# Optimization experiments

Measured on AMD Instinct MI355X. Metric: run time of the kernel, lower is better.

Reference implementation:

```python
import math
import jax, jax.numpy as jnp
import numpy as np

R, K, H = 512, 250, 4      # num_ranges, top-K per range, heads
E = 16                     # embed_dim*2 (MHA width), head_dim = 4
LN_EPS = 1e-5


def _layernorm(x, g, b):
    mu = jnp.mean(x, axis=-1, keepdims=True)
    var = jnp.mean(jnp.square(x - mu), axis=-1, keepdims=True)
    return (x - mu) * jax.lax.rsqrt(var + LN_EPS) * g + b


def setup_inputs() -> dict:
    key = jax.random.key(0)
    ks = jax.random.split(key, 12)
    L = 2  # num_layers
    s = 0.02
    return {
        "power_vals": jax.random.normal(ks[0], (R * K, 8), jnp.float32),
        "ele_indices": jax.random.randint(ks[1], (R * K,), 0, 37),
        "azi_indices": jax.random.randint(ks[2], (R * K,), 0, 107),
        "vp_w": jax.random.normal(ks[3], (8, 8), jnp.float32) * s,      # values_project: Linear(8, embed_dim=8)
        "vp_b": jnp.zeros((8,), jnp.float32),
        "ele_emb": jax.random.normal(ks[4], (37, 4), jnp.float32) * s,  # Embedding(37, embed_dim//2)
        "azi_emb": jax.random.normal(ks[5], (107, 4), jnp.float32) * s, # Embedding(107, embed_dim//2)
        "in_proj_w": jax.random.normal(ks[6], (L, 3 * E, E), jnp.float32) * s,
        "in_proj_b": jnp.zeros((L, 3 * E), jnp.float32),
        "out_w": jax.random.normal(ks[7], (L, E, E), jnp.float32) * s,
        "out_b": jnp.zeros((L, E), jnp.float32),
        "ln_g": jnp.ones((E,), jnp.float32),
        "ln_b": jnp.zeros((E,), jnp.float32),
    }


def reference(power_vals, ele_indices, azi_indices, vp_w, vp_b, ele_emb, azi_emb,
              in_proj_w, in_proj_b, out_w, out_b, ln_g, ln_b):
    D = E // H
    scale = 1.0 / math.sqrt(D)
    pv = power_vals.reshape(R, K, 8)
    top_values = pv @ vp_w.T + vp_b                      # [R,K,8]
    ele = ele_emb[ele_indices.reshape(R, K)]             # [R,K,4]
    azi = azi_emb[azi_indices.reshape(R, K)]             # [R,K,4]
    x = jnp.concatenate([top_values, ele, azi], axis=-1) # [R,K,16]

    # eval mode: dropout (both in MHA and after norm) is identity
    for l in range(in_proj_w.shape[0]):
        qkv = x @ in_proj_w[l].T + in_proj_b[l]          # [R,K,48]
        q, k, v = jnp.split(qkv, 3, axis=-1)
        q = q.reshape(R, K, H, D) * scale
        k = k.reshape(R, K, H, D)
        v = v.reshape(R, K, H, D)
        att = jnp.einsum('rqhd,rkhd->rhqk', q, k)        # [R,H,K,K]
        p = jax.nn.softmax(att, axis=-1)
        o = jnp.einsum('rhqk,rkhd->rqhd', p, v).reshape(R, K, E)
        o = o @ out_w[l].T + out_b[l]                    # out_proj
        x = _layernorm(o + x, ln_g, ln_b)                # shared LayerNorm, residual
    return x.reshape(R * K, E)
```

## Files before the change

### kernel.cpp

```cpp
#include <hip/hip_runtime.h>

#define R_ 512
#define K_ 250
#define E_ 16
#define L_ 2
#define SX_S 20

#define SCALE_LOG2E 0.72134752044448170f

#define ATT_STEP(KP, VP) do {                                                        \
    const float4 k0 = ((const float4*)(KP))[0];                                      \
    const float4 k1 = ((const float4*)(KP))[1];                                      \
    const float4 k2 = ((const float4*)(KP))[2];                                      \
    const float4 k3 = ((const float4*)(KP))[3];                                      \
    float s00 = fmaf(q0[0],k0.x, fmaf(q0[1],k0.y, fmaf(q0[2],k0.z, q0[3]*k0.w)));    \
    float s01 = fmaf(q0[4],k1.x, fmaf(q0[5],k1.y, fmaf(q0[6],k1.z, q0[7]*k1.w)));    \
    float s02 = fmaf(q0[8],k2.x, fmaf(q0[9],k2.y, fmaf(q0[10],k2.z, q0[11]*k2.w)));  \
    float s03 = fmaf(q0[12],k3.x, fmaf(q0[13],k3.y, fmaf(q0[14],k3.z, q0[15]*k3.w)));\
    float s10 = fmaf(q1[0],k0.x, fmaf(q1[1],k0.y, fmaf(q1[2],k0.z, q1[3]*k0.w)));    \
    float s11 = fmaf(q1[4],k1.x, fmaf(q1[5],k1.y, fmaf(q1[6],k1.z, q1[7]*k1.w)));    \
    float s12 = fmaf(q1[8],k2.x, fmaf(q1[9],k2.y, fmaf(q1[10],k2.z, q1[11]*k2.w)));  \
    float s13 = fmaf(q1[12],k3.x, fmaf(q1[13],k3.y, fmaf(q1[14],k3.z, q1[15]*k3.w)));\
    const float p00 = __builtin_amdgcn_exp2f(s00);                                   \
    const float p01 = __builtin_amdgcn_exp2f(s01);                                   \
    const float p02 = __builtin_amdgcn_exp2f(s02);                                   \
    const float p03 = __builtin_amdgcn_exp2f(s03);                                   \
    const float p10 = __builtin_amdgcn_exp2f(s10);                                   \
    const float p11 = __builtin_amdgcn_exp2f(s11);                                   \
    const float p12 = __builtin_amdgcn_exp2f(s12);                                   \
    const float p13 = __builtin_amdgcn_exp2f(s13);                                   \
    const float4 v0 = ((const float4*)(VP))[0];                                      \
    const float4 v1 = ((const float4*)(VP))[1];                                      \
    const float4 v2 = ((const float4*)(VP))[2];                                      \
    const float4 v3 = ((const float4*)(VP))[3];                                      \
    ls0 += p00; ls1 += p01; ls2 += p02; ls3 += p03;                                  \
    ls4 += p10; ls5 += p11; ls6 += p12; ls7 += p13;                                  \
    acc0[0]  = fmaf(p00, v0.x, acc0[0]);  acc0[1]  = fmaf(p00, v0.y, acc0[1]);       \
    acc0[2]  = fmaf(p00, v0.z, acc0[2]);  acc0[3]  = fmaf(p00, v0.w, acc0[3]);       \
    acc0[4]  = fmaf(p01, v1.x, acc0[4]);  acc0[5]  = fmaf(p01, v1.y, acc0[5]);       \
    acc0[6]  = fmaf(p01, v1.z, acc0[6]);  acc0[7]  = fmaf(p01, v1.w, acc0[7]);       \
    acc0[8]  = fmaf(p02, v2.x, acc0[8]);  acc0[9]  = fmaf(p02, v2.y, acc0[9]);       \
    acc0[10] = fmaf(p02, v2.z, acc0[10]); acc0[11] = fmaf(p02, v2.w, acc0[11]);      \
    acc0[12] = fmaf(p03, v3.x, acc0[12]); acc0[13] = fmaf(p03, v3.y, acc0[13]);      \
    acc0[14] = fmaf(p03, v3.z, acc0[14]); acc0[15] = fmaf(p03, v3.w, acc0[15]);      \
    acc1[0]  = fmaf(p10, v0.x, acc1[0]);  acc1[1]  = fmaf(p10, v0.y, acc1[1]);       \
    acc1[2]  = fmaf(p10, v0.z, acc1[2]);  acc1[3]  = fmaf(p10, v0.w, acc1[3]);       \
    acc1[4]  = fmaf(p11, v1.x, acc1[4]);  acc1[5]  = fmaf(p11, v1.y, acc1[5]);       \
    acc1[6]  = fmaf(p11, v1.z, acc1[6]);  acc1[7]  = fmaf(p11, v1.w, acc1[7]);       \
    acc1[8]  = fmaf(p12, v2.x, acc1[8]);  acc1[9]  = fmaf(p12, v2.y, acc1[9]);       \
    acc1[10] = fmaf(p12, v2.z, acc1[10]); acc1[11] = fmaf(p12, v2.w, acc1[11]);      \
    acc1[12] = fmaf(p13, v3.x, acc1[12]); acc1[13] = fmaf(p13, v3.y, acc1[13]);      \
    acc1[14] = fmaf(p13, v3.z, acc1[14]); acc1[15] = fmaf(p13, v3.w, acc1[15]);      \
} while (0)

__global__ __launch_bounds__(512, 2)
void mlra_kernel(const float* __restrict__ pv,
                 const int*   __restrict__ ele_idx,
                 const int*   __restrict__ azi_idx,
                 const float* __restrict__ vp_w,
                 const float* __restrict__ vp_b,
                 const float* __restrict__ ele_emb,
                 const float* __restrict__ azi_emb,
                 const float* __restrict__ ipw,
                 const float* __restrict__ ipb,
                 const float* __restrict__ outw,
                 const float* __restrict__ outb,
                 const float* __restrict__ lng,
                 const float* __restrict__ lnb,
                 float* __restrict__ out)
{
    __shared__ float s_k[K_][16];
    __shared__ float s_v[K_][16];
    __shared__ float s_x[K_][SX_S];
    __shared__ float s_w[768];
    __shared__ float s_b[48];
    __shared__ float s_ow[256];
    __shared__ float s_ob[16];
    __shared__ float s_vpw[64];
    __shared__ float s_vpb[8];
    __shared__ float s_ele[148];
    __shared__ float s_azi[428];
    __shared__ float s_lng[16], s_lnb[16];

    const int r = blockIdx.x;
    const int t = threadIdx.x;

    if (t < 64) s_vpw[t] = vp_w[t];
    if (t < 8)  s_vpb[t] = vp_b[t];
    for (int i = t; i < 148; i += 512) s_ele[i] = ele_emb[i];
    for (int i = t; i < 428; i += 512) s_azi[i] = azi_emb[i];
    if (t < 16) { s_lng[t] = lng[t]; s_lnb[t] = lnb[t]; }
    __syncthreads();

    if (t < K_) {
        const size_t row = (size_t)r * K_ + t;
        const float4 p0 = ((const float4*)(pv + row * 8))[0];
        const float4 p1 = ((const float4*)(pv + row * 8))[1];
        const float a[8] = {p0.x,p0.y,p0.z,p0.w,p1.x,p1.y,p1.z,p1.w};
        float xr[16];
        #pragma unroll
        for (int o = 0; o < 8; ++o) {
            const float4 w0 = ((const float4*)&s_vpw[o*8])[0];
            const float4 w1 = ((const float4*)&s_vpw[o*8])[1];
            float s = s_vpb[o];
            s = fmaf(a[0],w0.x,s); s = fmaf(a[1],w0.y,s); s = fmaf(a[2],w0.z,s); s = fmaf(a[3],w0.w,s);
            s = fmaf(a[4],w1.x,s); s = fmaf(a[5],w1.y,s); s = fmaf(a[6],w1.z,s); s = fmaf(a[7],w1.w,s);
            xr[o] = s;
        }
        const int ei = ele_idx[row];
        const int ai = azi_idx[row];
        const float4 ee = *(const float4*)&s_ele[ei*4];
        const float4 ae = *(const float4*)&s_azi[ai*4];
        xr[8]=ee.x; xr[9]=ee.y; xr[10]=ee.z; xr[11]=ee.w;
        xr[12]=ae.x; xr[13]=ae.y; xr[14]=ae.z; xr[15]=ae.w;
        float4* xd = (float4*)&s_x[t][0];
        xd[0] = make_float4(xr[0],xr[1],xr[2],xr[3]);
        xd[1] = make_float4(xr[4],xr[5],xr[6],xr[7]);
        xd[2] = make_float4(xr[8],xr[9],xr[10],xr[11]);
        xd[3] = make_float4(xr[12],xr[13],xr[14],xr[15]);
    }

    const int  qp      = t >> 2;
    const int  quarter = t & 3;
    const bool act     = qp < 125;
    const int  q0row   = 2*qp;
    const int  q1row   = 2*qp + 1;
    const int  od      = 4*quarter;

    for (int l = 0; l < L_; ++l) {
        __syncthreads();
        for (int i = t; i < 768; i += 512) s_w[i] = ipw[l*768 + i];
        if (t < 48)  s_b[t]  = ipb[l*48 + t];
        if (t < 256) s_ow[t] = outw[l*256 + t];
        if (t < 16)  s_ob[t] = outb[l*16 + t];
        __syncthreads();

        float q0[16], q1[16];
        if (act) {
            float x0[16], x1[16];
            {
                const float4* xa = (const float4*)&s_x[q0row][0];
                const float4 a0 = xa[0], a1 = xa[1], a2 = xa[2], a3 = xa[3];
                x0[0]=a0.x; x0[1]=a0.y; x0[2]=a0.z; x0[3]=a0.w;
                x0[4]=a1.x; x0[5]=a1.y; x0[6]=a1.z; x0[7]=a1.w;
                x0[8]=a2.x; x0[9]=a2.y; x0[10]=a2.z; x0[11]=a2.w;
                x0[12]=a3.x; x0[13]=a3.y; x0[14]=a3.z; x0[15]=a3.w;
                const float4* xb = (const float4*)&s_x[q1row][0];
                const float4 b0 = xb[0], b1 = xb[1], b2 = xb[2], b3 = xb[3];
                x1[0]=b0.x; x1[1]=b0.y; x1[2]=b0.z; x1[3]=b0.w;
                x1[4]=b1.x; x1[5]=b1.y; x1[6]=b1.z; x1[7]=b1.w;
                x1[8]=b2.x; x1[9]=b2.y; x1[10]=b2.z; x1[11]=b2.w;
                x1[12]=b3.x; x1[13]=b3.y; x1[14]=b3.z; x1[15]=b3.w;
            }
            #pragma unroll
            for (int o = 0; o < 16; ++o) {
                const float4 w0 = ((const float4*)&s_w[o*16])[0];
                const float4 w1 = ((const float4*)&s_w[o*16])[1];
                const float4 w2 = ((const float4*)&s_w[o*16])[2];
                const float4 w3 = ((const float4*)&s_w[o*16])[3];
                const float b = s_b[o];
                float a0 = b, a1 = b;
                a0=fmaf(x0[0],w0.x,a0); a0=fmaf(x0[1],w0.y,a0); a0=fmaf(x0[2],w0.z,a0); a0=fmaf(x0[3],w0.w,a0);
                a0=fmaf(x0[4],w1.x,a0); a0=fmaf(x0[5],w1.y,a0); a0=fmaf(x0[6],w1.z,a0); a0=fmaf(x0[7],w1.w,a0);
                a0=fmaf(x0[8],w2.x,a0); a0=fmaf(x0[9],w2.y,a0); a0=fmaf(x0[10],w2.z,a0); a0=fmaf(x0[11],w2.w,a0);
                a0=fmaf(x0[12],w3.x,a0); a0=fmaf(x0[13],w3.y,a0); a0=fmaf(x0[14],w3.z,a0); a0=fmaf(x0[15],w3.w,a0);
                a1=fmaf(x1[0],w0.x,a1); a1=fmaf(x1[1],w0.y,a1); a1=fmaf(x1[2],w0.z,a1); a1=fmaf(x1[3],w0.w,a1);
                a1=fmaf(x1[4],w1.x,a1); a1=fmaf(x1[5],w1.y,a1); a1=fmaf(x1[6],w1.z,a1); a1=fmaf(x1[7],w1.w,a1);
                a1=fmaf(x1[8],w2.x,a1); a1=fmaf(x1[9],w2.y,a1); a1=fmaf(x1[10],w2.z,a1); a1=fmaf(x1[11],w2.w,a1);
                a1=fmaf(x1[12],w3.x,a1); a1=fmaf(x1[13],w3.y,a1); a1=fmaf(x1[14],w3.z,a1); a1=fmaf(x1[15],w3.w,a1);
                q0[o] = a0 * SCALE_LOG2E;
                q1[o] = a1 * SCALE_LOG2E;
            }
            float xs[16];
            #pragma unroll
            for (int i = 0; i < 16; ++i) xs[i] = (quarter & 1) ? x1[i] : x0[i];
            const int kvb = (quarter < 2) ? 16 : 32;
            float kv[16];
            #pragma unroll
            for (int o = 0; o < 16; ++o) {
                const float* wr = &s_w[(kvb + o)*16];
                const float4 w0 = ((const float4*)wr)[0];
                const float4 w1 = ((const float4*)wr)[1];
                const float4 w2 = ((const float4*)wr)[2];
                const float4 w3 = ((const float4*)wr)[3];
                float s = s_b[kvb + o];
                s=fmaf(xs[0],w0.x,s); s=fmaf(xs[1],w0.y,s); s=fmaf(xs[2],w0.z,s); s=fmaf(xs[3],w0.w,s);
                s=fmaf(xs[4],w1.x,s); s=fmaf(xs[5],w1.y,s); s=fmaf(xs[6],w1.z,s); s=fmaf(xs[7],w1.w,s);
                s=fmaf(xs[8],w2.x,s); s=fmaf(xs[9],w2.y,s); s=fmaf(xs[10],w2.z,s); s=fmaf(xs[11],w2.w,s);
                s=fmaf(xs[12],w3.x,s); s=fmaf(xs[13],w3.y,s); s=fmaf(xs[14],w3.z,s); s=fmaf(xs[15],w3.w,s);
                kv[o] = s;
            }
            float* dst = ((quarter < 2) ? &s_k[0][0] : &s_v[0][0]) + (q0row + (quarter & 1))*16;
            ((float4*)dst)[0] = make_float4(kv[0],kv[1],kv[2],kv[3]);
            ((float4*)dst)[1] = make_float4(kv[4],kv[5],kv[6],kv[7]);
            ((float4*)dst)[2] = make_float4(kv[8],kv[9],kv[10],kv[11]);
            ((float4*)dst)[3] = make_float4(kv[12],kv[13],kv[14],kv[15]);
        }
        __syncthreads();

        if (act) {
            float acc0[16], acc1[16];
            #pragma unroll
            for (int i = 0; i < 16; ++i) { acc0[i] = 0.0f; acc1[i] = 0.0f; }
            float ls0=0.f, ls1=0.f, ls2=0.f, ls3=0.f, ls4=0.f, ls5=0.f, ls6=0.f, ls7=0.f;

            const float* kp  = &s_k[quarter][0];
            const float* vp2 = &s_v[quarter][0];
            #pragma unroll 2
            for (int jj = 0; jj < 62; ++jj) {
                ATT_STEP(kp, vp2);
                kp += 64; vp2 += 64;
            }
            if (quarter < 2) {
                ATT_STEP(kp, vp2);
            }

            #pragma unroll
            for (int i = 0; i < 16; ++i) {
                acc0[i] += __shfl_xor(acc0[i], 1);
                acc1[i] += __shfl_xor(acc1[i], 1);
            }
            ls0 += __shfl_xor(ls0,1); ls1 += __shfl_xor(ls1,1);
            ls2 += __shfl_xor(ls2,1); ls3 += __shfl_xor(ls3,1);
            ls4 += __shfl_xor(ls4,1); ls5 += __shfl_xor(ls5,1);
            ls6 += __shfl_xor(ls6,1); ls7 += __shfl_xor(ls7,1);
            #pragma unroll
            for (int i = 0; i < 16; ++i) {
                acc0[i] += __shfl_xor(acc0[i], 2);
                acc1[i] += __shfl_xor(acc1[i], 2);
            }
            ls0 += __shfl_xor(ls0,2); ls1 += __shfl_xor(ls1,2);
            ls2 += __shfl_xor(ls2,2); ls3 += __shfl_xor(ls3,2);
            ls4 += __shfl_xor(ls4,2); ls5 += __shfl_xor(ls5,2);
            ls6 += __shfl_xor(ls6,2); ls7 += __shfl_xor(ls7,2);

            const float i00 = __builtin_amdgcn_rcpf(ls0);
            const float i01 = __builtin_amdgcn_rcpf(ls1);
            const float i02 = __builtin_amdgcn_rcpf(ls2);
            const float i03 = __builtin_amdgcn_rcpf(ls3);
            const float i10 = __builtin_amdgcn_rcpf(ls4);
            const float i11 = __builtin_amdgcn_rcpf(ls5);
            const float i12 = __builtin_amdgcn_rcpf(ls6);
            const float i13 = __builtin_amdgcn_rcpf(ls7);
            float o0[16], o1[16];
            o0[0]=acc0[0]*i00;  o0[1]=acc0[1]*i00;  o0[2]=acc0[2]*i00;  o0[3]=acc0[3]*i00;
            o0[4]=acc0[4]*i01;  o0[5]=acc0[5]*i01;  o0[6]=acc0[6]*i01;  o0[7]=acc0[7]*i01;
            o0[8]=acc0[8]*i02;  o0[9]=acc0[9]*i02;  o0[10]=acc0[10]*i02; o0[11]=acc0[11]*i02;
            o0[12]=acc0[12]*i03; o0[13]=acc0[13]*i03; o0[14]=acc0[14]*i03; o0[15]=acc0[15]*i03;
            o1[0]=acc1[0]*i10;  o1[1]=acc1[1]*i10;  o1[2]=acc1[2]*i10;  o1[3]=acc1[3]*i10;
            o1[4]=acc1[4]*i11;  o1[5]=acc1[5]*i11;  o1[6]=acc1[6]*i11;  o1[7]=acc1[7]*i11;
            o1[8]=acc1[8]*i12;  o1[9]=acc1[9]*i12;  o1[10]=acc1[10]*i12; o1[11]=acc1[11]*i12;
            o1[12]=acc1[12]*i13; o1[13]=acc1[13]*i13; o1[14]=acc1[14]*i13; o1[15]=acc1[15]*i13;

            float y0[4], y1[4];
            #pragma unroll
            for (int c = 0; c < 4; ++c) {
                const float* wr = &s_ow[(od + c)*16];
                const float4 w0 = ((const float4*)wr)[0];
                const float4 w1 = ((const float4*)wr)[1];
                const float4 w2 = ((const float4*)wr)[2];
                const float4 w3 = ((const float4*)wr)[3];
                const float b = s_ob[od + c];
                float a0 = b, a1 = b;
                a0=fmaf(o0[0],w0.x,a0); a0=fmaf(o0[1],w0.y,a0); a0=fmaf(o0[2],w0.z,a0); a0=fmaf(o0[3],w0.w,a0);
                a0=fmaf(o0[4],w1.x,a0); a0=fmaf(o0[5],w1.y,a0); a0=fmaf(o0[6],w1.z,a0); a0=fmaf(o0[7],w1.w,a0);
                a0=fmaf(o0[8],w2.x,a0); a0=fmaf(o0[9],w2.y,a0); a0=fmaf(o0[10],w2.z,a0); a0=fmaf(o0[11],w2.w,a0);
                a0=fmaf(o0[12],w3.x,a0); a0=fmaf(o0[13],w3.y,a0); a0=fmaf(o0[14],w3.z,a0); a0=fmaf(o0[15],w3.w,a0);
                a1=fmaf(o1[0],w0.x,a1); a1=fmaf(o1[1],w0.y,a1); a1=fmaf(o1[2],w0.z,a1); a1=fmaf(o1[3],w0.w,a1);
                a1=fmaf(o1[4],w1.x,a1); a1=fmaf(o1[5],w1.y,a1); a1=fmaf(o1[6],w1.z,a1); a1=fmaf(o1[7],w1.w,a1);
                a1=fmaf(o1[8],w2.x,a1); a1=fmaf(o1[9],w2.y,a1); a1=fmaf(o1[10],w2.z,a1); a1=fmaf(o1[11],w2.w,a1);
                a1=fmaf(o1[12],w3.x,a1); a1=fmaf(o1[13],w3.y,a1); a1=fmaf(o1[14],w3.z,a1); a1=fmaf(o1[15],w3.w,a1);
                y0[c] = a0; y1[c] = a1;
            }
            const float4 xr0 = *(const float4*)&s_x[q0row][od];
            const float4 xr1 = *(const float4*)&s_x[q1row][od];
            const float t00 = y0[0]+xr0.x, t01 = y0[1]+xr0.y, t02 = y0[2]+xr0.z, t03 = y0[3]+xr0.w;
            const float t10 = y1[0]+xr1.x, t11 = y1[1]+xr1.y, t12 = y1[2]+xr1.z, t13 = y1[3]+xr1.w;
            float sum0 = (t00+t01)+(t02+t03);
            float sq0  = fmaf(t00,t00, fmaf(t01,t01, fmaf(t02,t02, t03*t03)));
            float sum1 = (t10+t11)+(t12+t13);
            float sq1  = fmaf(t10,t10, fmaf(t11,t11, fmaf(t12,t12, t13*t13)));
            sum0 += __shfl_xor(sum0,1); sum0 += __shfl_xor(sum0,2);
            sq0  += __shfl_xor(sq0,1);  sq0  += __shfl_xor(sq0,2);
            sum1 += __shfl_xor(sum1,1); sum1 += __shfl_xor(sum1,2);
            sq1  += __shfl_xor(sq1,1);  sq1  += __shfl_xor(sq1,2);
            const float mu0 = sum0 * 0.0625f;
            const float mu1 = sum1 * 0.0625f;
            const float var0 = fmaf(-mu0, mu0, sq0 * 0.0625f);
            const float var1 = fmaf(-mu1, mu1, sq1 * 0.0625f);
            const float rs0 = __builtin_amdgcn_rsqf(var0 + 1e-5f);
            const float rs1 = __builtin_amdgcn_rsqf(var1 + 1e-5f);
            const float4 g  = *(const float4*)&s_lng[od];
            const float4 bb = *(const float4*)&s_lnb[od];
            float4 xn0, xn1;
            xn0.x = (t00-mu0)*rs0*g.x + bb.x;  xn0.y = (t01-mu0)*rs0*g.y + bb.y;
            xn0.z = (t02-mu0)*rs0*g.z + bb.z;  xn0.w = (t03-mu0)*rs0*g.w + bb.w;
            xn1.x = (t10-mu1)*rs1*g.x + bb.x;  xn1.y = (t11-mu1)*rs1*g.y + bb.y;
            xn1.z = (t12-mu1)*rs1*g.z + bb.z;  xn1.w = (t13-mu1)*rs1*g.w + bb.w;
            *(float4*)&s_x[q0row][od] = xn0;
            *(float4*)&s_x[q1row][od] = xn1;
            if (l == L_ - 1) {
                float* ob = out + ((size_t)r*K_ + q0row)*16 + od;
                *(float4*)ob        = xn0;
                *(float4*)(ob + 16) = xn1;
            }
        }
    }
}

extern "C" void kernel_launch(void* const* d_in, const int* in_sizes, int n_in,
                              void* d_out, int out_size, void* d_ws, size_t ws_size,
                              hipStream_t stream) {
    const float* pv      = (const float*)d_in[0];
    const int*   ele_idx = (const int*)  d_in[1];
    const int*   azi_idx = (const int*)  d_in[2];
    const float* vp_w    = (const float*)d_in[3];
    const float* vp_b    = (const float*)d_in[4];
    const float* ele_emb = (const float*)d_in[5];
    const float* azi_emb = (const float*)d_in[6];
    const float* ipw     = (const float*)d_in[7];
    const float* ipb     = (const float*)d_in[8];
    const float* outw    = (const float*)d_in[9];
    const float* outb    = (const float*)d_in[10];
    const float* lng     = (const float*)d_in[11];
    const float* lnb     = (const float*)d_in[12];
    float* out = (float*)d_out;

    mlra_kernel<<<R_, 512, 0, stream>>>(pv, ele_idx, azi_idx, vp_w, vp_b,
                                        ele_emb, azi_emb, ipw, ipb,
                                        outw, outb, lng, lnb, out);
}
```

Before: 189.1 us.

## Split layers into two launches, each range split across two blocks

The single fused kernel, with one block per range looping over both layers, becomes two templated launches, one per layer, passing activations through a workspace buffer. Each range now gets two blocks that each own half the queries, and both blocks recompute K and V for the whole range. Eight threads share each query pair instead of four, with a wider shuffle reduction. This raises block count and per-query parallelism at the cost of redundant K/V projection, an extra global round trip for the activations, and a second launch.

```diff
diff --git a/kernel.cpp b/kernel.cpp
--- a/kernel.cpp
+++ b/kernel.cpp
@@ -2,10 +2,7 @@
 
 #define R_ 512
 #define K_ 250
-#define E_ 16
-#define L_ 2
-#define SX_S 20
-
+#define SK 20
 #define SCALE_LOG2E 0.72134752044448170f
 
 #define ATT_STEP(KP, VP) do {                                                        \
@@ -53,25 +50,27 @@
     acc1[14] = fmaf(p13, v3.z, acc1[14]); acc1[15] = fmaf(p13, v3.w, acc1[15]);      \
 } while (0)
 
+template<int PASS>
 __global__ __launch_bounds__(512, 2)
-void mlra_kernel(const float* __restrict__ pv,
-                 const int*   __restrict__ ele_idx,
-                 const int*   __restrict__ azi_idx,
-                 const float* __restrict__ vp_w,
-                 const float* __restrict__ vp_b,
-                 const float* __restrict__ ele_emb,
-                 const float* __restrict__ azi_emb,
-                 const float* __restrict__ ipw,
-                 const float* __restrict__ ipb,
-                 const float* __restrict__ outw,
-                 const float* __restrict__ outb,
-                 const float* __restrict__ lng,
-                 const float* __restrict__ lnb,
-                 float* __restrict__ out)
+void mlra_pass(const float* __restrict__ pv,
+               const int*   __restrict__ ele_idx,
+               const int*   __restrict__ azi_idx,
+               const float* __restrict__ vp_w,
+               const float* __restrict__ vp_b,
+               const float* __restrict__ ele_emb,
+               const float* __restrict__ azi_emb,
+               const float* __restrict__ ipw,
+               const float* __restrict__ ipb,
+               const float* __restrict__ outw,
+               const float* __restrict__ outb,
+               const float* __restrict__ lng,
+               const float* __restrict__ lnb,
+               const float* __restrict__ xin,
+               float* __restrict__ xout)
 {
-    __shared__ float s_k[K_][16];
-    __shared__ float s_v[K_][16];
-    __shared__ float s_x[K_][SX_S];
+    __shared__ float s_k[K_][SK];
+    __shared__ float s_v[K_][SK];
+    __shared__ float s_x[252][SK];
     __shared__ float s_w[768];
     __shared__ float s_b[48];
     __shared__ float s_ow[256];
@@ -82,228 +81,238 @@
     __shared__ float s_azi[428];
     __shared__ float s_lng[16], s_lnb[16];
 
-    const int r = blockIdx.x;
+    const int r = blockIdx.x >> 1;
+    const int s = blockIdx.x & 1;
     const int t = threadIdx.x;
 
-    if (t < 64) s_vpw[t] = vp_w[t];
-    if (t < 8)  s_vpb[t] = vp_b[t];
-    for (int i = t; i < 148; i += 512) s_ele[i] = ele_emb[i];
-    for (int i = t; i < 428; i += 512) s_azi[i] = azi_emb[i];
-    if (t < 16) { s_lng[t] = lng[t]; s_lnb[t] = lnb[t]; }
+    for (int i = t; i < 768; i += 512) s_w[i] = ipw[PASS*768 + i];
+    if (t < 48)  s_b[t]  = ipb[PASS*48 + t];
+    if (t < 256) s_ow[t] = outw[PASS*256 + t];
+    if (t < 16)  s_ob[t] = outb[PASS*16 + t];
+    if (t < 16)  { s_lng[t] = lng[t]; s_lnb[t] = lnb[t]; }
+    if (PASS == 0) {
+        if (t >= 64 && t < 128) s_vpw[t-64] = vp_w[t-64];
+        if (t >= 128 && t < 136) s_vpb[t-128] = vp_b[t-128];
+        for (int i = t; i < 148; i += 512) s_ele[i] = ele_emb[i];
+        for (int i = t; i < 428; i += 512) s_azi[i] = azi_emb[i];
+    }
     __syncthreads();
 
     if (t < K_) {
-        const size_t row = (size_t)r * K_ + t;
-        const float4 p0 = ((const float4*)(pv + row * 8))[0];
-        const float4 p1 = ((const float4*)(pv + row * 8))[1];
-        const float a[8] = {p0.x,p0.y,p0.z,p0.w,p1.x,p1.y,p1.z,p1.w};
         float xr[16];
-        #pragma unroll
-        for (int o = 0; o < 8; ++o) {
-            const float4 w0 = ((const float4*)&s_vpw[o*8])[0];
-            const float4 w1 = ((const float4*)&s_vpw[o*8])[1];
-            float s = s_vpb[o];
-            s = fmaf(a[0],w0.x,s); s = fmaf(a[1],w0.y,s); s = fmaf(a[2],w0.z,s); s = fmaf(a[3],w0.w,s);
-            s = fmaf(a[4],w1.x,s); s = fmaf(a[5],w1.y,s); s = fmaf(a[6],w1.z,s); s = fmaf(a[7],w1.w,s);
-            xr[o] = s;
-        }
-        const int ei = ele_idx[row];
-        const int ai = azi_idx[row];
-        const float4 ee = *(const float4*)&s_ele[ei*4];
-        const float4 ae = *(const float4*)&s_azi[ai*4];
-        xr[8]=ee.x; xr[9]=ee.y; xr[10]=ee.z; xr[11]=ee.w;
-        xr[12]=ae.x; xr[13]=ae.y; xr[14]=ae.z; xr[15]=ae.w;
+        if (PASS == 0) {
+            const size_t row = (size_t)r * K_ + t;
+            const float4 p0 = ((const float4*)(pv + row * 8))[0];
+            const float4 p1 = ((const float4*)(pv + row * 8))[1];
+            const float a[8] = {p0.x,p0.y,p0.z,p0.w,p1.x,p1.y,p1.z,p1.w};
+            #pragma unroll
+            for (int o = 0; o < 8; ++o) {
+                const float4 w0 = ((const float4*)&s_vpw[o*8])[0];
+                const float4 w1 = ((const float4*)&s_vpw[o*8])[1];
+                float sv = s_vpb[o];
+                sv = fmaf(a[0],w0.x,sv); sv = fmaf(a[1],w0.y,sv); sv = fmaf(a[2],w0.z,sv); sv = fmaf(a[3],w0.w,sv);
+                sv = fmaf(a[4],w1.x,sv); sv = fmaf(a[5],w1.y,sv); sv = fmaf(a[6],w1.z,sv); sv = fmaf(a[7],w1.w,sv);
+                xr[o] = sv;
+            }
+            const int ei = ele_idx[row];
+            const int ai = azi_idx[row];
+            const float4 ee = *(const float4*)&s_ele[ei*4];
+            const float4 ae = *(const float4*)&s_azi[ai*4];
+            xr[8]=ee.x; xr[9]=ee.y; xr[10]=ee.z; xr[11]=ee.w;
+            xr[12]=ae.x; xr[13]=ae.y; xr[14]=ae.z; xr[15]=ae.w;
+        } else {
+            const float4* src = (const float4*)(xin + ((size_t)r * K_ + t) * 16);
+            const float4 a0 = src[0], a1 = src[1], a2 = src[2], a3 = src[3];
+            xr[0]=a0.x; xr[1]=a0.y; xr[2]=a0.z; xr[3]=a0.w;
+            xr[4]=a1.x; xr[5]=a1.y; xr[6]=a1.z; xr[7]=a1.w;
+            xr[8]=a2.x; xr[9]=a2.y; xr[10]=a2.z; xr[11]=a2.w;
+            xr[12]=a3.x; xr[13]=a3.y; xr[14]=a3.z; xr[15]=a3.w;
+        }
         float4* xd = (float4*)&s_x[t][0];
         xd[0] = make_float4(xr[0],xr[1],xr[2],xr[3]);
         xd[1] = make_float4(xr[4],xr[5],xr[6],xr[7]);
         xd[2] = make_float4(xr[8],xr[9],xr[10],xr[11]);
         xd[3] = make_float4(xr[12],xr[13],xr[14],xr[15]);
-    }
-
-    const int  qp      = t >> 2;
-    const int  quarter = t & 3;
-    const bool act     = qp < 125;
-    const int  q0row   = 2*qp;
-    const int  q1row   = 2*qp + 1;
-    const int  od      = 4*quarter;
-
-    for (int l = 0; l < L_; ++l) {
-        __syncthreads();
-        for (int i = t; i < 768; i += 512) s_w[i] = ipw[l*768 + i];
-        if (t < 48)  s_b[t]  = ipb[l*48 + t];
-        if (t < 256) s_ow[t] = outw[l*256 + t];
-        if (t < 16)  s_ob[t] = outb[l*16 + t];
-        __syncthreads();
-
-        float q0[16], q1[16];
-        if (act) {
-            float x0[16], x1[16];
-            {
-                const float4* xa = (const float4*)&s_x[q0row][0];
-                const float4 a0 = xa[0], a1 = xa[1], a2 = xa[2], a3 = xa[3];
-                x0[0]=a0.x; x0[1]=a0.y; x0[2]=a0.z; x0[3]=a0.w;
-                x0[4]=a1.x; x0[5]=a1.y; x0[6]=a1.z; x0[7]=a1.w;
-                x0[8]=a2.x; x0[9]=a2.y; x0[10]=a2.z; x0[11]=a2.w;
-                x0[12]=a3.x; x0[13]=a3.y; x0[14]=a3.z; x0[15]=a3.w;
-                const float4* xb = (const float4*)&s_x[q1row][0];
-                const float4 b0 = xb[0], b1 = xb[1], b2 = xb[2], b3 = xb[3];
-                x1[0]=b0.x; x1[1]=b0.y; x1[2]=b0.z; x1[3]=b0.w;
-                x1[4]=b1.x; x1[5]=b1.y; x1[6]=b1.z; x1[7]=b1.w;
-                x1[8]=b2.x; x1[9]=b2.y; x1[10]=b2.z; x1[11]=b2.w;
-                x1[12]=b3.x; x1[13]=b3.y; x1[14]=b3.z; x1[15]=b3.w;
-            }
-            #pragma unroll
-            for (int o = 0; o < 16; ++o) {
-                const float4 w0 = ((const float4*)&s_w[o*16])[0];
-                const float4 w1 = ((const float4*)&s_w[o*16])[1];
-                const float4 w2 = ((const float4*)&s_w[o*16])[2];
-                const float4 w3 = ((const float4*)&s_w[o*16])[3];
-                const float b = s_b[o];
-                float a0 = b, a1 = b;
-                a0=fmaf(x0[0],w0.x,a0); a0=fmaf(x0[1],w0.y,a0); a0=fmaf(x0[2],w0.z,a0); a0=fmaf(x0[3],w0.w,a0);
-                a0=fmaf(x0[4],w1.x,a0); a0=fmaf(x0[5],w1.y,a0); a0=fmaf(x0[6],w1.z,a0); a0=fmaf(x0[7],w1.w,a0);
-                a0=fmaf(x0[8],w2.x,a0); a0=fmaf(x0[9],w2.y,a0); a0=fmaf(x0[10],w2.z,a0); a0=fmaf(x0[11],w2.w,a0);
-                a0=fmaf(x0[12],w3.x,a0); a0=fmaf(x0[13],w3.y,a0); a0=fmaf(x0[14],w3.z,a0); a0=fmaf(x0[15],w3.w,a0);
-                a1=fmaf(x1[0],w0.x,a1); a1=fmaf(x1[1],w0.y,a1); a1=fmaf(x1[2],w0.z,a1); a1=fmaf(x1[3],w0.w,a1);
-                a1=fmaf(x1[4],w1.x,a1); a1=fmaf(x1[5],w1.y,a1); a1=fmaf(x1[6],w1.z,a1); a1=fmaf(x1[7],w1.w,a1);
-                a1=fmaf(x1[8],w2.x,a1); a1=fmaf(x1[9],w2.y,a1); a1=fmaf(x1[10],w2.z,a1); a1=fmaf(x1[11],w2.w,a1);
-                a1=fmaf(x1[12],w3.x,a1); a1=fmaf(x1[13],w3.y,a1); a1=fmaf(x1[14],w3.z,a1); a1=fmaf(x1[15],w3.w,a1);
-                q0[o] = a0 * SCALE_LOG2E;
-                q1[o] = a1 * SCALE_LOG2E;
-            }
-            float xs[16];
-            #pragma unroll
-            for (int i = 0; i < 16; ++i) xs[i] = (quarter & 1) ? x1[i] : x0[i];
-            const int kvb = (quarter < 2) ? 16 : 32;
+    } else if (t < 252 + 6) {
+        if (t >= 256 && t < 258) {
+            float4* xd = (float4*)&s_x[250 + (t - 256)][0];
+            xd[0] = xd[1] = xd[2] = xd[3] = make_float4(0.f,0.f,0.f,0.f);
+        }
+    }
+    __syncthreads();
+
+    const int  qp    = t >> 3;
+    const int  e     = t & 7;
+    const bool qact  = qp < 63;
+    const int  qbase = s * 125;
+    const int  arow  = qbase + 2*qp;
+    const int  brow  = arow + 1;
+    const bool bval  = brow < K_;
+    const int  od    = 2*e;
+
+    float q0[16], q1[16];
+    if (qact) {
+        float x0[16], x1[16];
+        {
+            const float4* xa = (const float4*)&s_x[arow][0];
+            const float4 a0 = xa[0], a1 = xa[1], a2 = xa[2], a3 = xa[3];
+            x0[0]=a0.x; x0[1]=a0.y; x0[2]=a0.z; x0[3]=a0.w;
+            x0[4]=a1.x; x0[5]=a1.y; x0[6]=a1.z; x0[7]=a1.w;
+            x0[8]=a2.x; x0[9]=a2.y; x0[10]=a2.z; x0[11]=a2.w;
+            x0[12]=a3.x; x0[13]=a3.y; x0[14]=a3.z; x0[15]=a3.w;
+            const float4* xb = (const float4*)&s_x[brow][0];
+            const float4 b0 = xb[0], b1 = xb[1], b2 = xb[2], b3 = xb[3];
+            x1[0]=b0.x; x1[1]=b0.y; x1[2]=b0.z; x1[3]=b0.w;
+            x1[4]=b1.x; x1[5]=b1.y; x1[6]=b1.z; x1[7]=b1.w;
+            x1[8]=b2.x; x1[9]=b2.y; x1[10]=b2.z; x1[11]=b2.w;
+            x1[12]=b3.x; x1[13]=b3.y; x1[14]=b3.z; x1[15]=b3.w;
+        }
+        #pragma unroll
+        for (int o = 0; o < 16; ++o) {
+            const float4 w0 = ((const float4*)&s_w[o*16])[0];
+            const float4 w1 = ((const float4*)&s_w[o*16])[1];
+            const float4 w2 = ((const float4*)&s_w[o*16])[2];
+            const float4 w3 = ((const float4*)&s_w[o*16])[3];
+            const float b = s_b[o];
+            float a0 = b, a1 = b;
+            a0=fmaf(x0[0],w0.x,a0); a0=fmaf(x0[1],w0.y,a0); a0=fmaf(x0[2],w0.z,a0); a0=fmaf(x0[3],w0.w,a0);
+            a0=fmaf(x0[4],w1.x,a0); a0=fmaf(x0[5],w1.y,a0); a0=fmaf(x0[6],w1.z,a0); a0=fmaf(x0[7],w1.w,a0);
+            a0=fmaf(x0[8],w2.x,a0); a0=fmaf(x0[9],w2.y,a0); a0=fmaf(x0[10],w2.z,a0); a0=fmaf(x0[11],w2.w,a0);
+            a0=fmaf(x0[12],w3.x,a0); a0=fmaf(x0[13],w3.y,a0); a0=fmaf(x0[14],w3.z,a0); a0=fmaf(x0[15],w3.w,a0);
+            a1=fmaf(x1[0],w0.x,a1); a1=fmaf(x1[1],w0.y,a1); a1=fmaf(x1[2],w0.z,a1); a1=fmaf(x1[3],w0.w,a1);
+            a1=fmaf(x1[4],w1.x,a1); a1=fmaf(x1[5],w1.y,a1); a1=fmaf(x1[6],w1.z,a1); a1=fmaf(x1[7],w1.w,a1);
+            a1=fmaf(x1[8],w2.x,a1); a1=fmaf(x1[9],w2.y,a1); a1=fmaf(x1[10],w2.z,a1); a1=fmaf(x1[11],w2.w,a1);
+            a1=fmaf(x1[12],w3.x,a1); a1=fmaf(x1[13],w3.y,a1); a1=fmaf(x1[14],w3.z,a1); a1=fmaf(x1[15],w3.w,a1);
+            q0[o] = a0 * SCALE_LOG2E;
+            q1[o] = a1 * SCALE_LOG2E;
+        }
+    }
+    {
+        int kvrow = -1, base = 16;
+        if (t < K_)                        { kvrow = t;       base = 16; }
+        else if (t >= 256 && t < 256 + K_) { kvrow = t - 256; base = 32; }
+        if (kvrow >= 0) {
+            const float4* xs4 = (const float4*)&s_x[kvrow][0];
+            const float4 a0 = xs4[0], a1 = xs4[1], a2 = xs4[2], a3 = xs4[3];
+            const float xs[16] = {a0.x,a0.y,a0.z,a0.w, a1.x,a1.y,a1.z,a1.w,
+                                  a2.x,a2.y,a2.z,a2.w, a3.x,a3.y,a3.z,a3.w};
             float kv[16];
             #pragma unroll
             for (int o = 0; o < 16; ++o) {
-                const float* wr = &s_w[(kvb + o)*16];
+                const float* wr = &s_w[(base + o)*16];
                 const float4 w0 = ((const float4*)wr)[0];
                 const float4 w1 = ((const float4*)wr)[1];
                 const float4 w2 = ((const float4*)wr)[2];
                 const float4 w3 = ((const float4*)wr)[3];
-                float s = s_b[kvb + o];
-                s=fmaf(xs[0],w0.x,s); s=fmaf(xs[1],w0.y,s); s=fmaf(xs[2],w0.z,s); s=fmaf(xs[3],w0.w,s);
-                s=fmaf(xs[4],w1.x,s); s=fmaf(xs[5],w1.y,s); s=fmaf(xs[6],w1.z,s); s=fmaf(xs[7],w1.w,s);
-                s=fmaf(xs[8],w2.x,s); s=fmaf(xs[9],w2.y,s); s=fmaf(xs[10],w2.z,s); s=fmaf(xs[11],w2.w,s);
-                s=fmaf(xs[12],w3.x,s); s=fmaf(xs[13],w3.y,s); s=fmaf(xs[14],w3.z,s); s=fmaf(xs[15],w3.w,s);
-                kv[o] = s;
+                float sv = s_b[base + o];
+                sv=fmaf(xs[0],w0.x,sv); sv=fmaf(xs[1],w0.y,sv); sv=fmaf(xs[2],w0.z,sv); sv=fmaf(xs[3],w0.w,sv);
+                sv=fmaf(xs[4],w1.x,sv); sv=fmaf(xs[5],w1.y,sv); sv=fmaf(xs[6],w1.z,sv); sv=fmaf(xs[7],w1.w,sv);
+                sv=fmaf(xs[8],w2.x,sv); sv=fmaf(xs[9],w2.y,sv); sv=fmaf(xs[10],w2.z,sv); sv=fmaf(xs[11],w2.w,sv);
+                sv=fmaf(xs[12],w3.x,sv); sv=fmaf(xs[13],w3.y,sv); sv=fmaf(xs[14],w3.z,sv); sv=fmaf(xs[15],w3.w,sv);
+                kv[o] = sv;
             }
-            float* dst = ((quarter < 2) ? &s_k[0][0] : &s_v[0][0]) + (q0row + (quarter & 1))*16;
+            float* dst = (base == 16) ? &s_k[kvrow][0] : &s_v[kvrow][0];
             ((float4*)dst)[0] = make_float4(kv[0],kv[1],kv[2],kv[3]);
             ((float4*)dst)[1] = make_float4(kv[4],kv[5],kv[6],kv[7]);
             ((float4*)dst)[2] = make_float4(kv[8],kv[9],kv[10],kv[11]);
             ((float4*)dst)[3] = make_float4(kv[12],kv[13],kv[14],kv[15]);
         }
-        __syncthreads();
-
-        if (act) {
-            float acc0[16], acc1[16];
-            #pragma unroll
-            for (int i = 0; i < 16; ++i) { acc0[i] = 0.0f; acc1[i] = 0.0f; }
-            float ls0=0.f, ls1=0.f, ls2=0.f, ls3=0.f, ls4=0.f, ls5=0.f, ls6=0.f, ls7=0.f;
-
-            const float* kp  = &s_k[quarter][0];
-            const float* vp2 = &s_v[quarter][0];
-            #pragma unroll 2
-            for (int jj = 0; jj < 62; ++jj) {
-                ATT_STEP(kp, vp2);
-                kp += 64; vp2 += 64;
-            }
-            if (quarter < 2) {
-                ATT_STEP(kp, vp2);
-            }
-
+    }
+    __syncthreads();
+
+    if (qact) {
+        float acc0[16], acc1[16];
+        #pragma unroll
+        for (int i = 0; i < 16; ++i) { acc0[i] = 0.0f; acc1[i] = 0.0f; }
+        float ls0=0.f, ls1=0.f, ls2=0.f, ls3=0.f, ls4=0.f, ls5=0.f, ls6=0.f, ls7=0.f;
+
+        const float* kp  = &s_k[e][0];
+        const float* vp2 = &s_v[e][0];
+        const int n = 31 + ((e < 2) ? 1 : 0);
+        #pragma unroll 2
+        for (int jj = 0; jj < n; ++jj) {
+            ATT_STEP(kp, vp2);
+            kp += 8*SK; vp2 += 8*SK;
+        }
+
+        #pragma unroll
+        for (int m = 1; m <= 4; m <<= 1) {
             #pragma unroll
             for (int i = 0; i < 16; ++i) {
-                acc0[i] += __shfl_xor(acc0[i], 1);
-                acc1[i] += __shfl_xor(acc1[i], 1);
+                acc0[i] += __shfl_xor(acc0[i], m);
+                acc1[i] += __shfl_xor(acc1[i], m);
             }
-            ls0 += __shfl_xor(ls0,1); ls1 += __shfl_xor(ls1,1);
-            ls2 += __shfl_xor(ls2,1); ls3 += __shfl_xor(ls3,1);
-            ls4 += __shfl_xor(ls4,1); ls5 += __shfl_xor(ls5,1);
-            ls6 += __shfl_xor(ls6,1); ls7 += __shfl_xor(ls7,1);
-            #pragma unroll
-            for (int i = 0; i < 16; ++i) {
-                acc0[i] += __shfl_xor(acc0[i], 2);
-                acc1[i] += __shfl_xor(acc1[i], 2);
-            }
-            ls0 += __shfl_xor(ls0,2); ls1 += __shfl_xor(ls1,2);
-            ls2 += __shfl_xor(ls2,2); ls3 += __shfl_xor(ls3,2);
-            ls4 += __shfl_xor(ls4,2); ls5 += __shfl_xor(ls5,2);
-            ls6 += __shfl_xor(ls6,2); ls7 += __shfl_xor(ls7,2);
-
-            const float i00 = __builtin_amdgcn_rcpf(ls0);
-            const float i01 = __builtin_amdgcn_rcpf(ls1);
-            const float i02 = __builtin_amdgcn_rcpf(ls2);
-            const float i03 = __builtin_amdgcn_rcpf(ls3);
-            const float i10 = __builtin_amdgcn_rcpf(ls4);
-            const float i11 = __builtin_amdgcn_rcpf(ls5);
-            const float i12 = __builtin_amdgcn_rcpf(ls6);
-            const float i13 = __builtin_amdgcn_rcpf(ls7);
-            float o0[16], o1[16];
-            o0[0]=acc0[0]*i00;  o0[1]=acc0[1]*i00;  o0[2]=acc0[2]*i00;  o0[3]=acc0[3]*i00;
-            o0[4]=acc0[4]*i01;  o0[5]=acc0[5]*i01;  o0[6]=acc0[6]*i01;  o0[7]=acc0[7]*i01;
-            o0[8]=acc0[8]*i02;  o0[9]=acc0[9]*i02;  o0[10]=acc0[10]*i02; o0[11]=acc0[11]*i02;
-            o0[12]=acc0[12]*i03; o0[13]=acc0[13]*i03; o0[14]=acc0[14]*i03; o0[15]=acc0[15]*i03;
-            o1[0]=acc1[0]*i10;  o1[1]=acc1[1]*i10;  o1[2]=acc1[2]*i10;  o1[3]=acc1[3]*i10;
-            o1[4]=acc1[4]*i11;  o1[5]=acc1[5]*i11;  o1[6]=acc1[6]*i11;  o1[7]=acc1[7]*i11;
-            o1[8]=acc1[8]*i12;  o1[9]=acc1[9]*i12;  o1[10]=acc1[10]*i12; o1[11]=acc1[11]*i12;
-            o1[12]=acc1[12]*i13; o1[13]=acc1[13]*i13; o1[14]=acc1[14]*i13; o1[15]=acc1[15]*i13;
-
-            float y0[4], y1[4];
-            #pragma unroll
-            for (int c = 0; c < 4; ++c) {
-                const float* wr = &s_ow[(od + c)*16];
-                const float4 w0 = ((const float4*)wr)[0];
-                const float4 w1 = ((const float4*)wr)[1];
-                const float4 w2 = ((const float4*)wr)[2];
-                const float4 w3 = ((const float4*)wr)[3];
-                const float b = s_ob[od + c];
-                float a0 = b, a1 = b;
-                a0=fmaf(o0[0],w0.x,a0); a0=fmaf(o0[1],w0.y,a0); a0=fmaf(o0[2],w0.z,a0); a0=fmaf(o0[3],w0.w,a0);
-                a0=fmaf(o0[4],w1.x,a0); a0=fmaf(o0[5],w1.y,a0); a0=fmaf(o0[6],w1.z,a0); a0=fmaf(o0[7],w1.w,a0);
-                a0=fmaf(o0[8],w2.x,a0); a0=fmaf(o0[9],w2.y,a0); a0=fmaf(o0[10],w2.z,a0); a0=fmaf(o0[11],w2.w,a0);
-                a0=fmaf(o0[12],w3.x,a0); a0=fmaf(o0[13],w3.y,a0); a0=fmaf(o0[14],w3.z,a0); a0=fmaf(o0[15],w3.w,a0);
-                a1=fmaf(o1[0],w0.x,a1); a1=fmaf(o1[1],w0.y,a1); a1=fmaf(o1[2],w0.z,a1); a1=fmaf(o1[3],w0.w,a1);
-                a1=fmaf(o1[4],w1.x,a1); a1=fmaf(o1[5],w1.y,a1); a1=fmaf(o1[6],w1.z,a1); a1=fmaf(o1[7],w1.w,a1);
-                a1=fmaf(o1[8],w2.x,a1); a1=fmaf(o1[9],w2.y,a1); a1=fmaf(o1[10],w2.z,a1); a1=fmaf(o1[11],w2.w,a1);
-                a1=fmaf(o1[12],w3.x,a1); a1=fmaf(o1[13],w3.y,a1); a1=fmaf(o1[14],w3.z,a1); a1=fmaf(o1[15],w3.w,a1);
-                y0[c] = a0; y1[c] = a1;
-            }
-            const float4 xr0 = *(const float4*)&s_x[q0row][od];
-            const float4 xr1 = *(const float4*)&s_x[q1row][od];
-            const float t00 = y0[0]+xr0.x, t01 = y0[1]+xr0.y, t02 = y0[2]+xr0.z, t03 = y0[3]+xr0.w;
-            const float t10 = y1[0]+xr1.x, t11 = y1[1]+xr1.y, t12 = y1[2]+xr1.z, t13 = y1[3]+xr1.w;
-            float sum0 = (t00+t01)+(t02+t03);
-            float sq0  = fmaf(t00,t00, fmaf(t01,t01, fmaf(t02,t02, t03*t03)));
-            float sum1 = (t10+t11)+(t12+t13);
-            float sq1  = fmaf(t10,t10, fmaf(t11,t11, fmaf(t12,t12, t13*t13)));
-            sum0 += __shfl_xor(sum0,1); sum0 += __shfl_xor(sum0,2);
-            sq0  += __shfl_xor(sq0,1);  sq0  += __shfl_xor(sq0,2);
-            sum1 += __shfl_xor(sum1,1); sum1 += __shfl_xor(sum1,2);
-            sq1  += __shfl_xor(sq1,1);  sq1  += __shfl_xor(sq1,2);
-            const float mu0 = sum0 * 0.0625f;
-            const float mu1 = sum1 * 0.0625f;
-            const float var0 = fmaf(-mu0, mu0, sq0 * 0.0625f);
-            const float var1 = fmaf(-mu1, mu1, sq1 * 0.0625f);
-            const float rs0 = __builtin_amdgcn_rsqf(var0 + 1e-5f);
-            const float rs1 = __builtin_amdgcn_rsqf(var1 + 1e-5f);
-            const float4 g  = *(const float4*)&s_lng[od];
-            const float4 bb = *(const float4*)&s_lnb[od];
-            float4 xn0, xn1;
-            xn0.x = (t00-mu0)*rs0*g.x + bb.x;  xn0.y = (t01-mu0)*rs0*g.y + bb.y;
-            xn0.z = (t02-mu0)*rs0*g.z + bb.z;  xn0.w = (t03-mu0)*rs0*g.w + bb.w;
-            xn1.x = (t10-mu1)*rs1*g.x + bb.x;  xn1.y = (t11-mu1)*rs1*g.y + bb.y;
-            xn1.z = (t12-mu1)*rs1*g.z + bb.z;  xn1.w = (t13-mu1)*rs1*g.w + bb.w;
-            *(float4*)&s_x[q0row][od] = xn0;
-            *(float4*)&s_x[q1row][od] = xn1;
-            if (l == L_ - 1) {
-                float* ob = out + ((size_t)r*K_ + q0row)*16 + od;
-                *(float4*)ob        = xn0;
-                *(float4*)(ob + 16) = xn1;
-            }
+            ls0 += __shfl_xor(ls0,m); ls1 += __shfl_xor(ls1,m);
+            ls2 += __shfl_xor(ls2,m); ls3 += __shfl_xor(ls3,m);
+            ls4 += __shfl_xor(ls4,m); ls5 += __shfl_xor(ls5,m);
+            ls6 += __shfl_xor(ls6,m); ls7 += __shfl_xor(ls7,m);
+        }
+
+        const float i00 = __builtin_amdgcn_rcpf(ls0);
+        const float i01 = __builtin_amdgcn_rcpf(ls1);
+        const float i02 = __builtin_amdgcn_rcpf(ls2);
+        const float i03 = __builtin_amdgcn_rcpf(ls3);
+        const float i10 = __builtin_amdgcn_rcpf(ls4);
+        const float i11 = __builtin_amdgcn_rcpf(ls5);
+        const float i12 = __builtin_amdgcn_rcpf(ls6);
+        const float i13 = __builtin_amdgcn_rcpf(ls7);
+        float o0[16], o1[16];
+        o0[0]=acc0[0]*i00;  o0[1]=acc0[1]*i00;  o0[2]=acc0[2]*i00;  o0[3]=acc0[3]*i00;
+        o0[4]=acc0[4]*i01;  o0[5]=acc0[5]*i01;  o0[6]=acc0[6]*i01;  o0[7]=acc0[7]*i01;
+        o0[8]=acc0[8]*i02;  o0[9]=acc0[9]*i02;  o0[10]=acc0[10]*i02; o0[11]=acc0[11]*i02;
+        o0[12]=acc0[12]*i03; o0[13]=acc0[13]*i03; o0[14]=acc0[14]*i03; o0[15]=acc0[15]*i03;
+        o1[0]=acc1[0]*i10;  o1[1]=acc1[1]*i10;  o1[2]=acc1[2]*i10;  o1[3]=acc1[3]*i10;
+        o1[4]=acc1[4]*i11;  o1[5]=acc1[5]*i11;  o1[6]=acc1[6]*i11;  o1[7]=acc1[7]*i11;
+        o1[8]=acc1[8]*i12;  o1[9]=acc1[9]*i12;  o1[10]=acc1[10]*i12; o1[11]=acc1[11]*i12;
+        o1[12]=acc1[12]*i13; o1[13]=acc1[13]*i13; o1[14]=acc1[14]*i13; o1[15]=acc1[15]*i13;
+
+        float y0[2], y1[2];
+        #pragma unroll
+        for (int c = 0; c < 2; ++c) {
+            const float* wr = &s_ow[(od + c)*16];
+            const float4 w0 = ((const float4*)wr)[0];
+            const float4 w1 = ((const float4*)wr)[1];
+            const float4 w2 = ((const float4*)wr)[2];
+            const float4 w3 = ((const float4*)wr)[3];
+            const float b = s_ob[od + c];
+            float a0 = b, a1 = b;
+            a0=fmaf(o0[0],w0.x,a0); a0=fmaf(o0[1],w0.y,a0); a0=fmaf(o0[2],w0.z,a0); a0=fmaf(o0[3],w0.w,a0);
+            a0=fmaf(o0[4],w1.x,a0); a0=fmaf(o0[5],w1.y,a0); a0=fmaf(o0[6],w1.z,a0); a0=fmaf(o0[7],w1.w,a0);
+            a0=fmaf(o0[8],w2.x,a0); a0=fmaf(o0[9],w2.y,a0); a0=fmaf(o0[10],w2.z,a0); a0=fmaf(o0[11],w2.w,a0);
+            a0=fmaf(o0[12],w3.x,a0); a0=fmaf(o0[13],w3.y,a0); a0=fmaf(o0[14],w3.z,a0); a0=fmaf(o0[15],w3.w,a0);
+            a1=fmaf(o1[0],w0.x,a1); a1=fmaf(o1[1],w0.y,a1); a1=fmaf(o1[2],w0.z,a1); a1=fmaf(o1[3],w0.w,a1);
+            a1=fmaf(o1[4],w1.x,a1); a1=fmaf(o1[5],w1.y,a1); a1=fmaf(o1[6],w1.z,a1); a1=fmaf(o1[7],w1.w,a1);
+            a1=fmaf(o1[8],w2.x,a1); a1=fmaf(o1[9],w2.y,a1); a1=fmaf(o1[10],w2.z,a1); a1=fmaf(o1[11],w2.w,a1);
+            a1=fmaf(o1[12],w3.x,a1); a1=fmaf(o1[13],w3.y,a1); a1=fmaf(o1[14],w3.z,a1); a1=fmaf(o1[15],w3.w,a1);
+            y0[c] = a0; y1[c] = a1;
+        }
+        const float2 xr0 = *(const float2*)&s_x[arow][od];
+        const float2 xr1 = *(const float2*)&s_x[brow][od];
+        const float t00 = y0[0]+xr0.x, t01 = y0[1]+xr0.y;
+        const float t10 = y1[0]+xr1.x, t11 = y1[1]+xr1.y;
+        float sum0 = t00+t01,               sum1 = t10+t11;
+        float sq0  = fmaf(t00,t00,t01*t01), sq1  = fmaf(t10,t10,t11*t11);
+        #pragma unroll
+        for (int m = 1; m <= 4; m <<= 1) {
+            sum0 += __shfl_xor(sum0,m); sq0 += __shfl_xor(sq0,m);
+            sum1 += __shfl_xor(sum1,m); sq1 += __shfl_xor(sq1,m);
+        }
+        const float mu0 = sum0 * 0.0625f;
+        const float mu1 = sum1 * 0.0625f;
+        const float var0 = fmaf(-mu0, mu0, sq0 * 0.0625f);
+        const float var1 = fmaf(-mu1, mu1, sq1 * 0.0625f);
+        const float rs0 = __builtin_amdgcn_rsqf(var0 + 1e-5f);
+        const float rs1 = __builtin_amdgcn_rsqf(var1 + 1e-5f);
+        const float2 g  = *(const float2*)&s_lng[od];
+        const float2 bb = *(const float2*)&s_lnb[od];
+        float2 xn0, xn1;
+        xn0.x = (t00-mu0)*rs0*g.x + bb.x;  xn0.y = (t01-mu0)*rs0*g.y + bb.y;
+        xn1.x = (t10-mu1)*rs1*g.x + bb.x;  xn1.y = (t11-mu1)*rs1*g.y + bb.y;
+        float* oa = xout + ((size_t)r*K_ + arow)*16 + od;
+        *(float2*)oa = xn0;
+        if (bval) {
+            float* ob = xout + ((size_t)r*K_ + brow)*16 + od;
+            *(float2*)ob = xn1;
         }
     }
 }
@@ -325,8 +334,12 @@
     const float* lng     = (const float*)d_in[11];
     const float* lnb     = (const float*)d_in[12];
     float* out = (float*)d_out;
-
-    mlra_kernel<<<R_, 512, 0, stream>>>(pv, ele_idx, azi_idx, vp_w, vp_b,
-                                        ele_emb, azi_emb, ipw, ipb,
-                                        outw, outb, lng, lnb, out);
+    float* xws = (float*)d_ws;
+
+    mlra_pass<0><<<2*R_, 512, 0, stream>>>(pv, ele_idx, azi_idx, vp_w, vp_b,
+                                           ele_emb, azi_emb, ipw, ipb,
+                                           outw, outb, lng, lnb, nullptr, xws);
+    mlra_pass<1><<<2*R_, 512, 0, stream>>>(pv, ele_idx, azi_idx, vp_w, vp_b,
+                                           ele_emb, azi_emb, ipw, ipb,
+                                           outw, outb, lng, lnb, xws, out);
 }
```

Measured after the change: 213.8 us. +13.1%, slower.
